# Optimization experiments

Measured on AMD Instinct MI355X. Metric: run time of the kernel, lower is better.

Reference implementation:

```python
import jax, jax.numpy as jnp
import numpy as np

N_POOL = 8  # init kwarg n

def setup_inputs() -> dict:
    key = jax.random.key(0)
    k1, k2 = jax.random.split(key)
    B, H, W, C = 8, 256, 512, 16
    FIL = 16  # must equal C for the final subtract to be shape-valid
    feature_map = jax.random.normal(k1, (B, H, W, C), dtype=jnp.float32)
    kernel = jax.random.normal(k2, (5, 5, C, FIL), dtype=jnp.float32) * 0.05  # HWIO
    bias = jnp.zeros((FIL,), dtype=jnp.float32)
    return {"feature_map": feature_map, "kernel": kernel, "bias": bias}


def _inpaint_rows(x, kernel_masked, bias):
    # x: [B, h, w, C]. Original builds, per output row r, a 5-row stack
    # [padded[r], 0, 0, 0, padded[r+4]] and runs a 5x5 valid conv.
    # Since rows 1..3 of the stack are zero, this equals a single 5x5 valid
    # conv over the zero-padded input with kernel rows 1..3 zeroed out.
    xp = jnp.pad(x, ((0, 0), (2, 2), (2, 2), (0, 0)))
    y = jax.lax.conv_general_dilated(
        xp, kernel_masked, window_strides=(1, 1), padding='VALID',
        dimension_numbers=('NHWC', 'HWIO', 'NHWC'))
    return jax.nn.relu(y + bias)


def reference(feature_map, kernel, bias):
    B, H, W, C = feature_map.shape
    FIL = kernel.shape[-1]
    n = N_POOL
    ph = H // n  # pool size along H (SAME == VALID since H % ph == 0)
    w2 = W // 2
    # AveragePooling2D(pool=(H/n, 2), strides same)
    out = feature_map.reshape(B, n, ph, w2, 2, C).mean(axis=(2, 4))  # [B,n,w2,C]

    row_mask = jnp.array([1.0, 0.0, 0.0, 0.0, 1.0], dtype=kernel.dtype)
    kernel_masked = kernel * row_mask[:, None, None, None]

    row_op = _inpaint_rows(out, kernel_masked, bias)  # [B,n,w2,FIL]
    col_op = jnp.transpose(
        _inpaint_rows(jnp.transpose(out, (0, 2, 1, 3)), kernel_masked, bias),
        (0, 2, 1, 3))  # [B,n,w2,FIL]

    row_up = jax.image.resize(row_op, (B, H, W, FIL), method='bilinear')
    col_up = jax.image.resize(col_op, (B, H, W, FIL), method='bilinear')

    stacked_op = jnp.concatenate([row_up, col_up], axis=3)        # [B,H,W,2*FIL]
    stacked_orig = jnp.concatenate([feature_map, feature_map], axis=3)
    diff = stacked_orig - stacked_op
    return jnp.concatenate([feature_map, diff], axis=3)          # [B,H,W,3*C]
```

## Files before the change

### kernel.cpp

```cpp
#include <hip/hip_runtime.h>

#define B 8
#define H 256
#define W 512
#define C 16
#define FIL 16
#define NP 8
#define PH 32
#define W2 256
#define CH 8
#define POOL_ELEMS (B*NP*W2*C)

typedef float f32x4 __attribute__((ext_vector_type(4)));

__global__ __launch_bounds__(256) void pool_kernel(const float* __restrict__ fm,
                                                   float* __restrict__ P) {
    int blk = blockIdx.x;
    int ch = blk & (CH - 1);
    int bi = blk >> 3;
    int t = threadIdx.x;
    const float4* src = (const float4*)fm + (size_t)bi * (PH * W * C / 4) + ch * 256 + t;
    float4 acc = make_float4(0.f, 0.f, 0.f, 0.f);
#pragma unroll 8
    for (int hh = 0; hh < PH; ++hh) {
        float4 v = src[hh * (W * C / 4)];
        acc.x += v.x; acc.y += v.y; acc.z += v.z; acc.w += v.w;
    }
    __shared__ float4 s[256];
    s[t] = acc;
    __syncthreads();
    if (t < 128) {
        int u = t >> 2, q = t & 3;
        float4 a = s[u * 8 + q], b2 = s[u * 8 + 4 + q];
        float4 r = make_float4((a.x + b2.x) * (1.0f / 64.0f),
                               (a.y + b2.y) * (1.0f / 64.0f),
                               (a.z + b2.z) * (1.0f / 64.0f),
                               (a.w + b2.w) * (1.0f / 64.0f));
        float4* out = (float4*)(P + (size_t)bi * (W2 * C)) + ch * 128 + t;
        *out = r;
    }
}

__global__ __launch_bounds__(256) void conv_kernel(const float* __restrict__ P,
                                                   const float* __restrict__ kern,
                                                   const float* __restrict__ bias,
                                                   float* __restrict__ ROW,
                                                   float* __restrict__ COL) {
    int blk = blockIdx.x;
    int part = blk & 3;
    int bi = blk >> 2;
    int b = bi >> 3, i = bi & 7;
    int t = threadIdx.x;
    __shared__ float K0[5 * C * FIL];
    __shared__ float K4[5 * C * FIL];
    for (int idx = t; idx < 5 * C * FIL; idx += 256) {
        K0[idx] = kern[idx];
        K4[idx] = kern[4 * 5 * C * FIL + idx];
    }
    __syncthreads();
    bool is_row = (part < 2);
    int jhalf = part & 1;
    int j = jhalf * 128 + (t >> 1);
    int fh = (t & 1) * 8;
    const float* Pb = P + (size_t)b * (NP * W2 * C);
    float acc[8];
#pragma unroll
    for (int f = 0; f < 8; ++f) acc[f] = bias[fh + f];

    if (is_row) {
#pragma unroll
        for (int rr = 0; rr < 2; ++rr) {
            int ii = i + (rr ? 2 : -2);
            if (ii < 0 || ii >= NP) continue;
            const float* Kr = (rr ? K4 : K0) + fh;
            for (int s = 0; s < 5; ++s) {
                int jj = j + s - 2;
                if (jj < 0 || jj >= W2) continue;
                const float4* p4 = (const float4*)(Pb + (size_t)(ii * W2 + jj) * C);
#pragma unroll
                for (int cq = 0; cq < 4; ++cq) {
                    float4 pv = p4[cq];
                    const float* kk = Kr + (s * C + cq * 4) * FIL;
#pragma unroll
                    for (int f = 0; f < 8; ++f) {
                        acc[f] = fmaf(pv.x, kk[f], acc[f]);
                        acc[f] = fmaf(pv.y, kk[FIL + f], acc[f]);
                        acc[f] = fmaf(pv.z, kk[2 * FIL + f], acc[f]);
                        acc[f] = fmaf(pv.w, kk[3 * FIL + f], acc[f]);
                    }
                }
            }
        }
        float* o = ROW + ((size_t)(b * NP + i) * W2 + j) * FIL + fh;
#pragma unroll
        for (int f = 0; f < 8; ++f) o[f] = fmaxf(acc[f], 0.0f);
    } else {
        for (int s = 0; s < 5; ++s) {
            int ii = i + s - 2;
            if (ii < 0 || ii >= NP) continue;
#pragma unroll
            for (int rr = 0; rr < 2; ++rr) {
                int jj = j + (rr ? 2 : -2);
                if (jj < 0 || jj >= W2) continue;
                const float* Kr = (rr ? K4 : K0) + fh;
                const float4* p4 = (const float4*)(Pb + (size_t)(ii * W2 + jj) * C);
#pragma unroll
                for (int cq = 0; cq < 4; ++cq) {
                    float4 pv = p4[cq];
                    const float* kk = Kr + (s * C + cq * 4) * FIL;
#pragma unroll
                    for (int f = 0; f < 8; ++f) {
                        acc[f] = fmaf(pv.x, kk[f], acc[f]);
                        acc[f] = fmaf(pv.y, kk[FIL + f], acc[f]);
                        acc[f] = fmaf(pv.z, kk[2 * FIL + f], acc[f]);
                        acc[f] = fmaf(pv.w, kk[3 * FIL + f], acc[f]);
                    }
                }
            }
        }
        float* o = COL + ((size_t)(b * NP + i) * W2 + j) * FIL + fh;
#pragma unroll
        for (int f = 0; f < 8; ++f) o[f] = fmaxf(acc[f], 0.0f);
    }
}

__global__ __launch_bounds__(384) void up_kernel(const float* __restrict__ fm,
                                                 const float* __restrict__ ROW,
                                                 const float* __restrict__ COL,
                                                 float* __restrict__ out) {
    int blk = blockIdx.x;
    int b = blk >> 8, h = blk & 255;
    int t = threadIdx.x;
    __shared__ float Rs[W2 * C];
    __shared__ float Cs[W2 * C];

    float sh = (h + 0.5f) * (1.0f / 32.0f) - 0.5f;
    float flh = floorf(sh);
    float fh = sh - flh;
    int i0 = (int)flh;
    int i1 = min(i0 + 1, NP - 1);
    i0 = max(i0, 0);
    float wa = 1.0f - fh, wb = fh;

    const float4* r0 = (const float4*)(ROW + (size_t)(b * NP + i0) * (W2 * C));
    const float4* r1 = (const float4*)(ROW + (size_t)(b * NP + i1) * (W2 * C));
    const float4* c0 = (const float4*)(COL + (size_t)(b * NP + i0) * (W2 * C));
    const float4* c1 = (const float4*)(COL + (size_t)(b * NP + i1) * (W2 * C));
    for (int idx = t; idx < W2 * C / 4; idx += 384) {
        float4 a = r0[idx], bv = r1[idx];
        ((float4*)Rs)[idx] = make_float4(wa * a.x + wb * bv.x, wa * a.y + wb * bv.y,
                                         wa * a.z + wb * bv.z, wa * a.w + wb * bv.w);
        float4 ca = c0[idx], cb = c1[idx];
        ((float4*)Cs)[idx] = make_float4(wa * ca.x + wb * cb.x, wa * ca.y + wb * cb.y,
                                         wa * ca.z + wb * cb.z, wa * ca.w + wb * cb.w);
    }
    __syncthreads();

    int p_local = t / 12;
    int q = t - p_local * 12;
    int cc = (q & 3) * 4;
    bool is_copy = (q < 4);
    const float* S = (q < 8) ? Rs : Cs;

    const float4* fmr = (const float4*)(fm + (size_t)(b * H + h) * (W * C));
    float4* orow = (float4*)(out + (size_t)(b * H + h) * (W * 48));
#pragma unroll
    for (int k = 0; k < 16; ++k) {
        int p = k * 32 + p_local;
        float4 v = fmr[p * 4 + (q & 3)];
        if (!is_copy) {
            float sw = 0.5f * p - 0.25f;
            float flw = floorf(sw);
            float fw = sw - flw;
            int j0i = max((int)flw, 0);
            int j1i = min((int)flw + 1, W2 - 1);
            const float* A  = S + j0i * 16 + cc;
            const float* Bv = S + j1i * 16 + cc;
            float iw = 1.0f - fw;
            v.x -= iw * A[0] + fw * Bv[0];
            v.y -= iw * A[1] + fw * Bv[1];
            v.z -= iw * A[2] + fw * Bv[2];
            v.w -= iw * A[3] + fw * Bv[3];
        }
        orow[(size_t)p * 12 + q] = v;
    }
}

extern "C" void kernel_launch(void* const* d_in, const int* in_sizes, int n_in,
                              void* d_out, int out_size, void* d_ws, size_t ws_size,
                              hipStream_t stream) {
    const float* fm   = (const float*)d_in[0];
    const float* kern = (const float*)d_in[1];
    const float* bias = (const float*)d_in[2];
    float* out = (float*)d_out;
    float* P   = (float*)d_ws;
    float* ROW = P + POOL_ELEMS;
    float* COL = ROW + POOL_ELEMS;

    pool_kernel<<<B * NP * CH, 256, 0, stream>>>(fm, P);
    conv_kernel<<<B * NP * 4, 256, 0, stream>>>(P, kern, bias, ROW, COL);
    up_kernel<<<B * H, 384, 0, stream>>>(fm, ROW, COL, out);
}
```

Measured before the change: 66.62 us.

## Split pooling over two row halves and remap up-kernel block order

The pooling kernel now launches twice as many blocks, each summing 16 of the 32 rows, and writes two partial pool buffers. The conv kernel adds the two partials when it loads its inputs. This gives the bandwidth-bound pool pass more parallelism and shorter per-thread dependency chains, at the cost of double the loads in the conv kernel and extra workspace. The up kernel also permutes blockIdx so consecutive blocks go to different batches, which changes how blocks are spread across XCDs and caches.

```diff
diff --git a/kernel.cpp b/kernel.cpp
--- a/kernel.cpp
+++ b/kernel.cpp
@@ -14,15 +14,17 @@
 typedef float f32x4 __attribute__((ext_vector_type(4)));
 
 __global__ __launch_bounds__(256) void pool_kernel(const float* __restrict__ fm,
-                                                   float* __restrict__ P) {
+                                                   float* __restrict__ PP) {
     int blk = blockIdx.x;
-    int ch = blk & (CH - 1);
-    int bi = blk >> 3;
+    int rh = blk & 1;
+    int ch = (blk >> 1) & (CH - 1);
+    int bi = blk >> 4;
     int t = threadIdx.x;
-    const float4* src = (const float4*)fm + (size_t)bi * (PH * W * C / 4) + ch * 256 + t;
+    const float4* src = (const float4*)fm + (size_t)bi * (PH * W * C / 4)
+                        + rh * 16 * (W * C / 4) + ch * 256 + t;
     float4 acc = make_float4(0.f, 0.f, 0.f, 0.f);
-#pragma unroll 8
-    for (int hh = 0; hh < PH; ++hh) {
+#pragma unroll 16
+    for (int hh = 0; hh < 16; ++hh) {
         float4 v = src[hh * (W * C / 4)];
         acc.x += v.x; acc.y += v.y; acc.z += v.z; acc.w += v.w;
     }
@@ -36,12 +38,13 @@
                                (a.y + b2.y) * (1.0f / 64.0f),
                                (a.z + b2.z) * (1.0f / 64.0f),
                                (a.w + b2.w) * (1.0f / 64.0f));
-        float4* out = (float4*)(P + (size_t)bi * (W2 * C)) + ch * 128 + t;
+        float4* out = (float4*)(PP + (size_t)rh * POOL_ELEMS + (size_t)bi * (W2 * C))
+                      + ch * 128 + t;
         *out = r;
     }
 }
 
-__global__ __launch_bounds__(256) void conv_kernel(const float* __restrict__ P,
+__global__ __launch_bounds__(256) void conv_kernel(const float* __restrict__ PP,
                                                    const float* __restrict__ kern,
                                                    const float* __restrict__ bias,
                                                    float* __restrict__ ROW,
@@ -62,7 +65,8 @@
     int jhalf = part & 1;
     int j = jhalf * 128 + (t >> 1);
     int fh = (t & 1) * 8;
-    const float* Pb = P + (size_t)b * (NP * W2 * C);
+    const float* Pb0 = PP + (size_t)b * (NP * W2 * C);
+    const float* Pb1 = Pb0 + POOL_ELEMS;
     float acc[8];
 #pragma unroll
     for (int f = 0; f < 8; ++f) acc[f] = bias[fh + f];
@@ -76,10 +80,13 @@
             for (int s = 0; s < 5; ++s) {
                 int jj = j + s - 2;
                 if (jj < 0 || jj >= W2) continue;
-                const float4* p4 = (const float4*)(Pb + (size_t)(ii * W2 + jj) * C);
+                const float4* p40 = (const float4*)(Pb0 + (size_t)(ii * W2 + jj) * C);
+                const float4* p41 = (const float4*)(Pb1 + (size_t)(ii * W2 + jj) * C);
 #pragma unroll
                 for (int cq = 0; cq < 4; ++cq) {
-                    float4 pv = p4[cq];
+                    float4 pa = p40[cq], pb = p41[cq];
+                    float4 pv = make_float4(pa.x + pb.x, pa.y + pb.y,
+                                            pa.z + pb.z, pa.w + pb.w);
                     const float* kk = Kr + (s * C + cq * 4) * FIL;
 #pragma unroll
                     for (int f = 0; f < 8; ++f) {
@@ -103,10 +110,13 @@
                 int jj = j + (rr ? 2 : -2);
                 if (jj < 0 || jj >= W2) continue;
                 const float* Kr = (rr ? K4 : K0) + fh;
-                const float4* p4 = (const float4*)(Pb + (size_t)(ii * W2 + jj) * C);
+                const float4* p40 = (const float4*)(Pb0 + (size_t)(ii * W2 + jj) * C);
+                const float4* p41 = (const float4*)(Pb1 + (size_t)(ii * W2 + jj) * C);
 #pragma unroll
                 for (int cq = 0; cq < 4; ++cq) {
-                    float4 pv = p4[cq];
+                    float4 pa = p40[cq], pb = p41[cq];
+                    float4 pv = make_float4(pa.x + pb.x, pa.y + pb.y,
+                                            pa.z + pb.z, pa.w + pb.w);
                     const float* kk = Kr + (s * C + cq * 4) * FIL;
 #pragma unroll
                     for (int f = 0; f < 8; ++f) {
@@ -128,7 +138,8 @@
                                                  const float* __restrict__ ROW,
                                                  const float* __restrict__ COL,
                                                  float* __restrict__ out) {
-    int blk = blockIdx.x;
+    int bid = blockIdx.x;
+    int blk = (bid & 7) * 256 + (bid >> 3);
     int b = blk >> 8, h = blk & 255;
     int t = threadIdx.x;
     __shared__ float Rs[W2 * C];
@@ -193,11 +204,11 @@
     const float* kern = (const float*)d_in[1];
     const float* bias = (const float*)d_in[2];
     float* out = (float*)d_out;
-    float* P   = (float*)d_ws;
-    float* ROW = P + POOL_ELEMS;
+    float* PP  = (float*)d_ws;
+    float* ROW = PP + 2 * POOL_ELEMS;
     float* COL = ROW + POOL_ELEMS;
 
-    pool_kernel<<<B * NP * CH, 256, 0, stream>>>(fm, P);
-    conv_kernel<<<B * NP * 4, 256, 0, stream>>>(P, kern, bias, ROW, COL);
+    pool_kernel<<<B * NP * CH * 2, 256, 0, stream>>>(fm, PP);
+    conv_kernel<<<B * NP * 4, 256, 0, stream>>>(PP, kern, bias, ROW, COL);
     up_kernel<<<B * H, 384, 0, stream>>>(fm, ROW, COL, out);
 }
```

New measurement: 67.05 us. Within noise of the previous version (+0.7%).
